# Kernel optimization log

Measured on AMD Instinct MI355X. Metric: run time of the kernel, lower is better.

## Reference

```python
import jax, jax.numpy as jnp
import numpy as np

N, E = 50000, 800000
IN_DIM, HID, OUT_DIM = 512, 64, 40


def setup_inputs() -> dict:
    key = jax.random.key(0)
    ks = jax.random.split(key, 7)
    X = jax.random.normal(ks[0], (N, IN_DIM), dtype=jnp.float32)
    edges = jax.random.randint(ks[1], (2, E), 0, N, dtype=jnp.int64)
    # GCNConv weight (glorot) and bias
    W1 = jax.random.normal(ks[2], (IN_DIM, HID), dtype=jnp.float32) / np.sqrt(IN_DIM)
    b1 = jnp.zeros((HID,), dtype=jnp.float32)
    # fc Linear
    Wfc = jax.random.normal(ks[3], (OUT_DIM, HID), dtype=jnp.float32) / np.sqrt(HID)
    bfc = jax.random.normal(ks[4], (OUT_DIM,), dtype=jnp.float32) * 0.01
    return {"X": X, "edges": edges, "W1": W1, "b1": b1, "Wfc": Wfc, "bfc": bfc}


def gcn_conv(x, src, dst, W, b, n):
    # PyG GCNConv: transform, add self-loops, symmetric D^-1/2 A D^-1/2 norm,
    # scatter-add messages at destination, add bias.
    h = x @ W  # [N, HID]
    loop = jnp.arange(n, dtype=src.dtype)
    src = jnp.concatenate([src, loop])
    dst = jnp.concatenate([dst, loop])
    deg = jax.ops.segment_sum(jnp.ones_like(dst, dtype=h.dtype), dst, num_segments=n)
    dinv = jnp.where(deg > 0, jax.lax.rsqrt(deg), 0.0)
    coef = dinv[src] * dinv[dst]  # [E+N]
    msgs = coef[:, None] * h[src]  # gather + scale
    agg = jax.ops.segment_sum(msgs, dst, num_segments=n)  # scatter-add
    return agg + b


def reference(X, edges, W1, b1, Wfc, bfc):
    n = X.shape[0]
    src, dst = edges[0], edges[1]
    h = jax.nn.relu(gcn_conv(X, src, dst, W1, b1, n))  # [N, HID]
    return h @ Wfc.T + bfc  # [N, OUT_DIM]
```

## Files before the change

### kernel.cpp

```cpp
#include <hip/hip_runtime.h>
#include <hip/hip_bf16.h>

typedef unsigned short u16;
typedef __bf16 bf16_8 __attribute__((ext_vector_type(8)));
typedef float f32_4 __attribute__((ext_vector_type(4)));

#define IN_DIM 512
#define HID 64
#define OUT_DIM 40
#define CAP 64
#define CF_BLOCKS 512

__global__ void k_prep(const float* __restrict__ W1, u16* __restrict__ W1t,
                       int* __restrict__ cnt, int n) {
    int i = blockIdx.x * 256 + threadIdx.x;
    if (i < n) cnt[i] = 0;
    if (i < IN_DIM * HID) {
        int k = i / HID, o = i % HID;
        __hip_bfloat16 v = __float2bfloat16(W1[i]);
        W1t[o * IN_DIM + k] = *reinterpret_cast<u16*>(&v);
    }
}

__launch_bounds__(256)
__global__ void k_work(const float* __restrict__ X, const u16* __restrict__ W1t,
                       const int* __restrict__ src, const int* __restrict__ dst,
                       int* cnt, u16* __restrict__ csr, u16* __restrict__ hs,
                       int N, int E, int NT) {
    __shared__ __align__(16) u16 As[2][64 * 40];
    const int t = threadIdx.x;

    if ((int)blockIdx.x >= NT) {
        int tid = ((int)blockIdx.x - NT) * 256 + t;
        int stride = CF_BLOCKS * 256;
        for (int e = tid; e < E; e += stride) {
            int d = dst[e];
            int p = atomicAdd(&cnt[d], 1);
            if (p < CAP) csr[(size_t)d * CAP + p] = (u16)src[e];
        }
        return;
    }

    const int wave = t >> 6;
    const int lane = t & 63;
    const int m = lane & 15;
    const int quad = lane >> 4;
    const int n0 = blockIdx.x * 64;

    f32_4 acc[4];
    #pragma unroll
    for (int c = 0; c < 4; c++) acc[c] = (f32_4){0.f, 0.f, 0.f, 0.f};

    const int r_st = t >> 2;
    const int k_st = (t & 3) * 8;

    int row = n0 + r_st; if (row >= N) row = N - 1;
    const float* xp = X + (size_t)row * IN_DIM + k_st;

    f32_4 x0 = *reinterpret_cast<const f32_4*>(xp);
    f32_4 x1 = *reinterpret_cast<const f32_4*>(xp + 4);

    int buf = 0;
    for (int k0 = 0; k0 < IN_DIM; k0 += 32) {
        u16 xb[8];
        #pragma unroll
        for (int q = 0; q < 4; q++) {
            __hip_bfloat16 c0 = __float2bfloat16(x0[q]);
            __hip_bfloat16 c1 = __float2bfloat16(x1[q]);
            xb[q]     = *reinterpret_cast<u16*>(&c0);
            xb[4 + q] = *reinterpret_cast<u16*>(&c1);
        }
        *reinterpret_cast<uint4*>(&As[buf][r_st * 40 + k_st]) = *reinterpret_cast<uint4*>(xb);
        __syncthreads();

        if (k0 + 32 < IN_DIM) {
            x0 = *reinterpret_cast<const f32_4*>(xp + k0 + 32);
            x1 = *reinterpret_cast<const f32_4*>(xp + k0 + 36);
        }

        bf16_8 a = *reinterpret_cast<const bf16_8*>(&As[buf][(wave * 16 + m) * 40 + quad * 8]);
        #pragma unroll
        for (int c = 0; c < 4; c++) {
            bf16_8 b = *reinterpret_cast<const bf16_8*>(
                W1t + (size_t)(c * 16 + m) * IN_DIM + k0 + quad * 8);
            acc[c] = __builtin_amdgcn_mfma_f32_16x16x32_bf16(a, b, acc[c], 0, 0, 0);
        }
        buf ^= 1;
    }

    const int nbase = n0 + wave * 16 + quad * 4;
    #pragma unroll
    for (int r = 0; r < 4; r++) {
        int n = nbase + r;
        if (n < N) {
            #pragma unroll
            for (int c = 0; c < 4; c++) {
                __hip_bfloat16 hv = __float2bfloat16(acc[c][r]);
                hs[(size_t)n * HID + c * 16 + m] = *reinterpret_cast<u16*>(&hv);
            }
        }
    }
}

__device__ __forceinline__ void cvt_accs(f32_4& a, uint2 v, float s) {
    a[0] += s * __uint_as_float(v.x << 16);
    a[1] += s * __uint_as_float(v.x & 0xFFFF0000u);
    a[2] += s * __uint_as_float(v.y << 16);
    a[3] += s * __uint_as_float(v.y & 0xFFFF0000u);
}

#define SHP 72

__launch_bounds__(256)
__global__ void k_aggfc(const u16* __restrict__ hs, const u16* __restrict__ csr,
                        const int* __restrict__ cnt, const float* __restrict__ b1,
                        const float* __restrict__ Wfc, const float* __restrict__ bfc,
                        float* __restrict__ out, int N) {
    __shared__ __align__(16) u16 shb[16 * SHP];
    __shared__ __align__(16) u16 wfb[48 * SHP];
    __shared__ float bl[48];
    const int t = threadIdx.x;

    for (int i = t; i < 48 * HID; i += 256) {
        int o = i / HID, k = i % HID;
        float v = (o < OUT_DIM) ? Wfc[o * HID + k] : 0.f;
        __hip_bfloat16 b = __float2bfloat16(v);
        wfb[o * SHP + k] = *reinterpret_cast<u16*>(&b);
    }
    if (t < 48) bl[t] = (t < OUT_DIM) ? bfc[t] : 0.f;

    const int g = t >> 4, l = t & 15;
    const int n = blockIdx.x * 16 + g;

    if (n < N) {
        const uint2* hs2 = reinterpret_cast<const uint2*>(hs);
        f32_4 a0 = (f32_4){0.f, 0.f, 0.f, 0.f};
        f32_4 a1 = a0, a2 = a0, a3 = a0;
        const float dvn = rsqrtf((float)cnt[n] + 1.0f);
        cvt_accs(a0, hs2[(size_t)n * 16 + l], dvn);
        int deg = cnt[n]; if (deg > CAP) deg = CAP;
        const u16* cs = csr + (size_t)n * CAP;
        int j = 0;
        for (; j + 7 < deg; j += 8) {
            int s0 = cs[j],     s1 = cs[j + 1], s2 = cs[j + 2], s3 = cs[j + 3];
            int s4 = cs[j + 4], s5 = cs[j + 5], s6 = cs[j + 6], s7 = cs[j + 7];
            float d0 = rsqrtf((float)cnt[s0] + 1.0f);
            float d1 = rsqrtf((float)cnt[s1] + 1.0f);
            float d2 = rsqrtf((float)cnt[s2] + 1.0f);
            float d3 = rsqrtf((float)cnt[s3] + 1.0f);
            float d4 = rsqrtf((float)cnt[s4] + 1.0f);
            float d5 = rsqrtf((float)cnt[s5] + 1.0f);
            float d6 = rsqrtf((float)cnt[s6] + 1.0f);
            float d7 = rsqrtf((float)cnt[s7] + 1.0f);
            uint2 v0 = hs2[(size_t)s0 * 16 + l];
            uint2 v1 = hs2[(size_t)s1 * 16 + l];
            uint2 v2 = hs2[(size_t)s2 * 16 + l];
            uint2 v3 = hs2[(size_t)s3 * 16 + l];
            uint2 v4 = hs2[(size_t)s4 * 16 + l];
            uint2 v5 = hs2[(size_t)s5 * 16 + l];
            uint2 v6 = hs2[(size_t)s6 * 16 + l];
            uint2 v7 = hs2[(size_t)s7 * 16 + l];
            cvt_accs(a0, v0, d0); cvt_accs(a1, v1, d1);
            cvt_accs(a2, v2, d2); cvt_accs(a3, v3, d3);
            cvt_accs(a0, v4, d4); cvt_accs(a1, v5, d5);
            cvt_accs(a2, v6, d6); cvt_accs(a3, v7, d7);
        }
        for (; j < deg; j++) {
            int s = cs[j];
            cvt_accs(a0, hs2[(size_t)s * 16 + l], rsqrtf((float)cnt[s] + 1.0f));
        }
        f32_4 acc = (a0 + a1) + (a2 + a3);
        u16 rb[4];
        #pragma unroll
        for (int q = 0; q < 4; q++) {
            float x = dvn * acc[q] + b1[l * 4 + q];
            x = x > 0.f ? x : 0.f;
            __hip_bfloat16 hb = __float2bfloat16(x);
            rb[q] = *reinterpret_cast<u16*>(&hb);
        }
        *reinterpret_cast<uint2*>(&shb[g * SHP + l * 4]) = *reinterpret_cast<uint2*>(rb);
    }
    __syncthreads();

    const int wave = t >> 6;
    const int lane = t & 63;
    const int m = lane & 15;
    const int quad = lane >> 4;
    if (wave < 3) {
        bf16_8 a0 = *reinterpret_cast<const bf16_8*>(&shb[m * SHP + quad * 8]);
        bf16_8 a1 = *reinterpret_cast<const bf16_8*>(&shb[m * SHP + 32 + quad * 8]);
        bf16_8 b0 = *reinterpret_cast<const bf16_8*>(&wfb[(wave * 16 + m) * SHP + quad * 8]);
        bf16_8 b1 = *reinterpret_cast<const bf16_8*>(&wfb[(wave * 16 + m) * SHP + 32 + quad * 8]);
        f32_4 c = (f32_4){0.f, 0.f, 0.f, 0.f};
        c = __builtin_amdgcn_mfma_f32_16x16x32_bf16(a0, b0, c, 0, 0, 0);
        c = __builtin_amdgcn_mfma_f32_16x16x32_bf16(a1, b1, c, 0, 0, 0);
        const int o = wave * 16 + m;
        if (o < OUT_DIM) {
            const int base = blockIdx.x * 16;
            #pragma unroll
            for (int r = 0; r < 4; r++) {
                int node = base + quad * 4 + r;
                if (node < N) out[(size_t)node * OUT_DIM + o] = c[r] + bl[o];
            }
        }
    }
}


extern "C" void kernel_launch(void* const* d_in, const int* in_sizes, int n_in,
                              void* d_out, int out_size, void* d_ws, size_t ws_size,
                              hipStream_t stream) {
    const float* X   = (const float*)d_in[0];
    const int* edges = (const int*)d_in[1];
    const float* W1  = (const float*)d_in[2];
    const float* b1  = (const float*)d_in[3];
    const float* Wfc = (const float*)d_in[4];
    const float* bfc = (const float*)d_in[5];

    const int N = in_sizes[0] / IN_DIM;
    const int E = in_sizes[1] / 2;
    const int* src = edges;
    const int* dst = edges + E;

    char* p = (char*)d_ws;
    auto carve = [&](size_t bytes) -> char* {
        char* r = p;
        p += (bytes + 255) & ~(size_t)255;
        return r;
    };
    u16* W1t = (u16*)carve((size_t)IN_DIM * HID * 2);
    u16* hs  = (u16*)carve((size_t)N * HID * 2);
    int* cnt = (int*)carve((size_t)N * 4);
    u16* csr = (u16*)carve((size_t)N * CAP * 2);

    const int nb = (N + 255) / 256;
    const int NT = (N + 63) / 64;

    k_prep <<<nb, 256, 0, stream>>>(W1, W1t, cnt, N);
    k_work <<<NT + CF_BLOCKS, 256, 0, stream>>>(X, W1t, src, dst, cnt, csr, hs, N, E, NT);
    k_aggfc<<<(N + 15) / 16, 256, 0, stream>>>(hs, csr, cnt, b1, Wfc, bfc,
                                               (float*)d_out, N);
}
```

Measured before the change: 235.8 us.

## Prescale h by source degree norm and load X directly into MFMA operands

Adds a k_scale pass that multiplies each row of hs by its own rsqrt(deg+1). This removes the per-edge random cnt[src] loads and rsqrt work from the aggregation loop. The GEMM now loads X straight from global memory into the MFMA A operand, dropping the shared-memory staging and per-step barriers. The CSR-fill blocks are moved to the front of the grid so they get scheduled first. The costs are an extra kernel launch, a read-write pass over hs, one extra bf16 rounding of the scaled values, and less coalesced X loads.

```diff
diff --git a/kernel.cpp b/kernel.cpp
--- a/kernel.cpp
+++ b/kernel.cpp
@@ -22,16 +22,27 @@
     }
 }
 
+__device__ __forceinline__ bf16_8 cvt8(f32_4 x0, f32_4 x1) {
+    u16 xb[8];
+    #pragma unroll
+    for (int q = 0; q < 4; q++) {
+        __hip_bfloat16 c0 = __float2bfloat16(x0[q]);
+        __hip_bfloat16 c1 = __float2bfloat16(x1[q]);
+        xb[q]     = *reinterpret_cast<u16*>(&c0);
+        xb[4 + q] = *reinterpret_cast<u16*>(&c1);
+    }
+    return *reinterpret_cast<bf16_8*>(xb);
+}
+
 __launch_bounds__(256)
 __global__ void k_work(const float* __restrict__ X, const u16* __restrict__ W1t,
                        const int* __restrict__ src, const int* __restrict__ dst,
                        int* cnt, u16* __restrict__ csr, u16* __restrict__ hs,
-                       int N, int E, int NT) {
-    __shared__ __align__(16) u16 As[2][64 * 40];
+                       int N, int E) {
     const int t = threadIdx.x;
 
-    if ((int)blockIdx.x >= NT) {
-        int tid = ((int)blockIdx.x - NT) * 256 + t;
+    if ((int)blockIdx.x < CF_BLOCKS) {
+        int tid = (int)blockIdx.x * 256 + t;
         int stride = CF_BLOCKS * 256;
         for (int e = tid; e < E; e += stride) {
             int d = dst[e];
@@ -41,51 +52,32 @@
         return;
     }
 
+    const int bid  = (int)blockIdx.x - CF_BLOCKS;
     const int wave = t >> 6;
     const int lane = t & 63;
-    const int m = lane & 15;
+    const int m    = lane & 15;
     const int quad = lane >> 4;
-    const int n0 = blockIdx.x * 64;
+    const int n0   = bid * 64;
+
+    int arow = n0 + wave * 16 + m;
+    if (arow >= N) arow = N - 1;
+    const float* xp = X + (size_t)arow * IN_DIM + quad * 8;
 
     f32_4 acc[4];
     #pragma unroll
     for (int c = 0; c < 4; c++) acc[c] = (f32_4){0.f, 0.f, 0.f, 0.f};
 
-    const int r_st = t >> 2;
-    const int k_st = (t & 3) * 8;
-
-    int row = n0 + r_st; if (row >= N) row = N - 1;
-    const float* xp = X + (size_t)row * IN_DIM + k_st;
-
-    f32_4 x0 = *reinterpret_cast<const f32_4*>(xp);
-    f32_4 x1 = *reinterpret_cast<const f32_4*>(xp + 4);
-
-    int buf = 0;
+    #pragma unroll 2
     for (int k0 = 0; k0 < IN_DIM; k0 += 32) {
-        u16 xb[8];
-        #pragma unroll
-        for (int q = 0; q < 4; q++) {
-            __hip_bfloat16 c0 = __float2bfloat16(x0[q]);
-            __hip_bfloat16 c1 = __float2bfloat16(x1[q]);
-            xb[q]     = *reinterpret_cast<u16*>(&c0);
-            xb[4 + q] = *reinterpret_cast<u16*>(&c1);
-        }
-        *reinterpret_cast<uint4*>(&As[buf][r_st * 40 + k_st]) = *reinterpret_cast<uint4*>(xb);
-        __syncthreads();
-
-        if (k0 + 32 < IN_DIM) {
-            x0 = *reinterpret_cast<const f32_4*>(xp + k0 + 32);
-            x1 = *reinterpret_cast<const f32_4*>(xp + k0 + 36);
-        }
-
-        bf16_8 a = *reinterpret_cast<const bf16_8*>(&As[buf][(wave * 16 + m) * 40 + quad * 8]);
+        f32_4 x0 = *reinterpret_cast<const f32_4*>(xp + k0);
+        f32_4 x1 = *reinterpret_cast<const f32_4*>(xp + k0 + 4);
+        bf16_8 a = cvt8(x0, x1);
         #pragma unroll
         for (int c = 0; c < 4; c++) {
             bf16_8 b = *reinterpret_cast<const bf16_8*>(
                 W1t + (size_t)(c * 16 + m) * IN_DIM + k0 + quad * 8);
             acc[c] = __builtin_amdgcn_mfma_f32_16x16x32_bf16(a, b, acc[c], 0, 0, 0);
         }
-        buf ^= 1;
     }
 
     const int nbase = n0 + wave * 16 + quad * 4;
@@ -102,11 +94,34 @@
     }
 }
 
-__device__ __forceinline__ void cvt_accs(f32_4& a, uint2 v, float s) {
-    a[0] += s * __uint_as_float(v.x << 16);
-    a[1] += s * __uint_as_float(v.x & 0xFFFF0000u);
-    a[2] += s * __uint_as_float(v.y << 16);
-    a[3] += s * __uint_as_float(v.y & 0xFFFF0000u);
+__global__ void k_scale(u16* __restrict__ hs, const int* __restrict__ cnt, int N) {
+    int idx = blockIdx.x * 256 + threadIdx.x;
+    int n = idx >> 4;
+    if (n < N) {
+        float dv = rsqrtf((float)cnt[n] + 1.0f);
+        uint2* p = reinterpret_cast<uint2*>(hs);
+        uint2 v = p[idx];
+        float f0 = __uint_as_float(v.x << 16) * dv;
+        float f1 = __uint_as_float(v.x & 0xFFFF0000u) * dv;
+        float f2 = __uint_as_float(v.y << 16) * dv;
+        float f3 = __uint_as_float(v.y & 0xFFFF0000u) * dv;
+        __hip_bfloat16 b0 = __float2bfloat16(f0);
+        __hip_bfloat16 b1 = __float2bfloat16(f1);
+        __hip_bfloat16 b2 = __float2bfloat16(f2);
+        __hip_bfloat16 b3 = __float2bfloat16(f3);
+        v.x = (unsigned)*reinterpret_cast<u16*>(&b0) |
+              ((unsigned)*reinterpret_cast<u16*>(&b1) << 16);
+        v.y = (unsigned)*reinterpret_cast<u16*>(&b2) |
+              ((unsigned)*reinterpret_cast<u16*>(&b3) << 16);
+        p[idx] = v;
+    }
+}
+
+__device__ __forceinline__ void cvt_acc(f32_4& a, uint2 v) {
+    a[0] += __uint_as_float(v.x << 16);
+    a[1] += __uint_as_float(v.x & 0xFFFF0000u);
+    a[2] += __uint_as_float(v.y << 16);
+    a[3] += __uint_as_float(v.y & 0xFFFF0000u);
 }
 
 #define SHP 72
@@ -136,22 +151,13 @@
         const uint2* hs2 = reinterpret_cast<const uint2*>(hs);
         f32_4 a0 = (f32_4){0.f, 0.f, 0.f, 0.f};
         f32_4 a1 = a0, a2 = a0, a3 = a0;
-        const float dvn = rsqrtf((float)cnt[n] + 1.0f);
-        cvt_accs(a0, hs2[(size_t)n * 16 + l], dvn);
+        cvt_acc(a0, hs2[(size_t)n * 16 + l]);
         int deg = cnt[n]; if (deg > CAP) deg = CAP;
         const u16* cs = csr + (size_t)n * CAP;
         int j = 0;
         for (; j + 7 < deg; j += 8) {
             int s0 = cs[j],     s1 = cs[j + 1], s2 = cs[j + 2], s3 = cs[j + 3];
             int s4 = cs[j + 4], s5 = cs[j + 5], s6 = cs[j + 6], s7 = cs[j + 7];
-            float d0 = rsqrtf((float)cnt[s0] + 1.0f);
-            float d1 = rsqrtf((float)cnt[s1] + 1.0f);
-            float d2 = rsqrtf((float)cnt[s2] + 1.0f);
-            float d3 = rsqrtf((float)cnt[s3] + 1.0f);
-            float d4 = rsqrtf((float)cnt[s4] + 1.0f);
-            float d5 = rsqrtf((float)cnt[s5] + 1.0f);
-            float d6 = rsqrtf((float)cnt[s6] + 1.0f);
-            float d7 = rsqrtf((float)cnt[s7] + 1.0f);
             uint2 v0 = hs2[(size_t)s0 * 16 + l];
             uint2 v1 = hs2[(size_t)s1 * 16 + l];
             uint2 v2 = hs2[(size_t)s2 * 16 + l];
@@ -160,16 +166,12 @@
             uint2 v5 = hs2[(size_t)s5 * 16 + l];
             uint2 v6 = hs2[(size_t)s6 * 16 + l];
             uint2 v7 = hs2[(size_t)s7 * 16 + l];
-            cvt_accs(a0, v0, d0); cvt_accs(a1, v1, d1);
-            cvt_accs(a2, v2, d2); cvt_accs(a3, v3, d3);
-            cvt_accs(a0, v4, d4); cvt_accs(a1, v5, d5);
-            cvt_accs(a2, v6, d6); cvt_accs(a3, v7, d7);
-        }
-        for (; j < deg; j++) {
-            int s = cs[j];
-            cvt_accs(a0, hs2[(size_t)s * 16 + l], rsqrtf((float)cnt[s] + 1.0f));
-        }
+            cvt_acc(a0, v0); cvt_acc(a1, v1); cvt_acc(a2, v2); cvt_acc(a3, v3);
+            cvt_acc(a0, v4); cvt_acc(a1, v5); cvt_acc(a2, v6); cvt_acc(a3, v7);
+        }
+        for (; j < deg; j++) cvt_acc(a0, hs2[(size_t)cs[j] * 16 + l]);
         f32_4 acc = (a0 + a1) + (a2 + a3);
+        const float dvn = rsqrtf((float)cnt[n] + 1.0f);
         u16 rb[4];
         #pragma unroll
         for (int q = 0; q < 4; q++) {
@@ -237,7 +239,8 @@
     const int NT = (N + 63) / 64;
 
     k_prep <<<nb, 256, 0, stream>>>(W1, W1t, cnt, N);
-    k_work <<<NT + CF_BLOCKS, 256, 0, stream>>>(X, W1t, src, dst, cnt, csr, hs, N, E, NT);
+    k_work <<<CF_BLOCKS + NT, 256, 0, stream>>>(X, W1t, src, dst, cnt, csr, hs, N, E);
+    k_scale<<<(N * 16 + 255) / 256, 256, 0, stream>>>(hs, cnt, N);
     k_aggfc<<<(N + 15) / 16, 256, 0, stream>>>(hs, csr, cnt, b1, Wfc, bfc,
                                                (float*)d_out, N);
 }
```

Result: slower. 249.0 us (+5.6%).
